# Optimization experiments

Measured on AMD Instinct MI355X. Metric: run time of the kernel, lower is better.

Reference implementation:

```python
import jax, jax.numpy as jnp
import numpy as np

N = 50000
E = 800000
IN_C = 128
HID = 32
OUT_C = 16
NEG_SLOPE = 0.2


def setup_inputs() -> dict:
    key = jax.random.key(0)
    ks = jax.random.split(key, 16)
    x = jax.random.normal(ks[0], (N, IN_C), dtype=jnp.float32)
    edge_index = jax.random.randint(ks[1], (2, E), 0, N, dtype=jnp.int64)

    def glorot(k, shape):
        fan = shape[0] + shape[-1]
        return jax.random.uniform(k, shape, jnp.float32, -1.0, 1.0) * jnp.sqrt(6.0 / fan)

    # layer1: in=128 -> heads=4, ch=32, concat -> out 128
    W1 = glorot(ks[2], (IN_C, 4 * HID))
    a_src1 = glorot(ks[3], (4, HID))
    a_dst1 = glorot(ks[4], (4, HID))
    b1 = jnp.zeros((4 * HID,), jnp.float32)
    # layer2: in=128 -> heads=2, ch=32, concat -> out 64
    W2 = glorot(ks[5], (4 * HID, 2 * HID))
    a_src2 = glorot(ks[6], (2, HID))
    a_dst2 = glorot(ks[7], (2, HID))
    b2 = jnp.zeros((2 * HID,), jnp.float32)
    # layer3: in=64 -> heads=1, ch=16, mean -> out 16
    W3 = glorot(ks[8], (2 * HID, OUT_C))
    a_src3 = glorot(ks[9], (1, OUT_C))
    a_dst3 = glorot(ks[10], (1, OUT_C))
    b3 = jnp.zeros((OUT_C,), jnp.float32)
    return {"x": x, "edge_index": edge_index,
            "W1": W1, "a_src1": a_src1, "a_dst1": a_dst1, "b1": b1,
            "W2": W2, "a_src2": a_src2, "a_dst2": a_dst2, "b2": b2,
            "W3": W3, "a_src3": a_src3, "a_dst3": a_dst3, "b3": b3}


def gat_conv(x, src, dst, W, a_src, a_dst, bias, heads, ch, concat):
    n = x.shape[0]
    h = (x @ W).reshape(n, heads, ch)                      # [N,H,C]
    alpha_s = jnp.einsum('nhc,hc->nh', h, a_src)           # [N,H]
    alpha_d = jnp.einsum('nhc,hc->nh', h, a_dst)           # [N,H]
    logits = jax.nn.leaky_relu(alpha_s[src] + alpha_d[dst], NEG_SLOPE)  # [E,H]
    # segment softmax over edges sharing the same destination node
    m = jax.ops.segment_max(logits, dst, num_segments=n)
    m = jnp.where(jnp.isfinite(m), m, 0.0)
    e = jnp.exp(logits - m[dst])
    denom = jax.ops.segment_sum(e, dst, num_segments=n)
    alpha = e / (denom[dst] + 1e-16)                       # [E,H]
    msg = h[src] * alpha[:, :, None]                       # [E,H,C]
    out = jax.ops.segment_sum(msg, dst, num_segments=n)    # [N,H,C]
    out = out.reshape(n, heads * ch) if concat else out.mean(axis=1)
    return out + bias


def reference(x, edge_index, W1, a_src1, a_dst1, b1, W2, a_src2, a_dst2, b2, W3, a_src3, a_dst3, b3):
    n = x.shape[0]
    loops = jnp.arange(n, dtype=edge_index.dtype)
    src = jnp.concatenate([edge_index[0], loops])  # add self loops (PyG default)
    dst = jnp.concatenate([edge_index[1], loops])
    h = jax.nn.relu(gat_conv(x, src, dst, W1, a_src1, a_dst1, b1, 4, HID, True))
    h = jax.nn.relu(gat_conv(h, src, dst, W2, a_src2, a_dst2, b2, 2, HID, True))
    out = gat_conv(h, src, dst, W3, a_src3, a_dst3, b3, 1, OUT_C, False)
    return out
```

## Files before the change

### kernel.cpp

```cpp
#include <hip/hip_runtime.h>
#include <hip/hip_bf16.h>
#include <stdint.h>

#define NODES 50000
#define NEDGE 800000
#define TEDGE (NEDGE + NODES)
#define SBLK 25
#define GBLK ((NODES + 63) / 64)
#define HBLK8 ((TEDGE + 2047) / 2048)
#define BL1_TOT (3 * HBLK8)

typedef unsigned short u16;
typedef unsigned int u32;
typedef unsigned long long u64;
typedef short s16x8 __attribute__((ext_vector_type(8)));
typedef float f32x4 __attribute__((ext_vector_type(4)));

__device__ __forceinline__ float bf2f(u16 v) {
  return __uint_as_float(((u32)v) << 16);
}
__device__ __forceinline__ u16 f2bf(float f) {
  u32 u = __float_as_uint(f);
  u32 r = (u + 0x7FFFu + ((u >> 16) & 1u)) >> 16;
  return (u16)r;
}
__device__ __forceinline__ float lo16f(u32 w) { return __uint_as_float(w << 16); }
__device__ __forceinline__ float hi16f(u32 w) { return __uint_as_float(w & 0xFFFF0000u); }
__device__ __forceinline__ float lrelu(float x) {
  return (x > 0.f) ? x : 0.2f * x;
}
__device__ __forceinline__ int clampn(int v) {
  return ((u32)v < NODES) ? v : 0;
}
__device__ __forceinline__ float load1(const void* p, size_t i, bool fb) {
  return fb ? bf2f(((const u16*)p)[i]) : ((const float*)p)[i];
}
__device__ __forceinline__ u32 encf(float f) {
  u32 u = __float_as_uint(f);
  return (u & 0x80000000u) ? ~u : (u | 0x80000000u);
}
__device__ __forceinline__ float decf(u32 k) {
  u32 u = (k & 0x80000000u) ? (k & 0x7FFFFFFFu) : ~k;
  return __uint_as_float(u);
}

__global__ __launch_bounds__(256) void k_probe(
    const int* __restrict__ ei, const u16* __restrict__ xs16,
    int* __restrict__ flags, int* __restrict__ deg,
    const void* __restrict__ W1, const void* __restrict__ W2,
    const void* __restrict__ W3, const void* __restrict__ as1,
    const void* __restrict__ ad1, const void* __restrict__ as2,
    const void* __restrict__ ad2, const void* __restrict__ as3,
    const void* __restrict__ ad3, u16* __restrict__ wt1,
    u16* __restrict__ wt2, u16* __restrict__ wt3, u16* __restrict__ wa1,
    u16* __restrict__ wa2, u16* __restrict__ wa3) {
  __shared__ int sfb;
  int t = threadIdx.x;
  int g = blockIdx.x * 256 + t;
  if (g < NODES) deg[g] = 0;
  if (blockIdx.x == 0 && t >= 2 && t < 32) flags[t] = 0;
  if (t < 64) {
    int big = 0;
#pragma unroll
    for (int k = 0; k < 4; ++k) {
      u32 ex = (xs16[2 * (t * 4 + k)] >> 7) & 0xFF;
      big += (ex >= 0x90);
    }
#pragma unroll
    for (int off = 32; off >= 1; off >>= 1) big += __shfl_xor(big, off);
    if (t == 0) sfb = (big >= 8) ? 0 : 1;
    if (blockIdx.x == 0) {
      int odd = 0, even = 0;
#pragma unroll
      for (int k = 0; k < 4; ++k) {
        int idx = t + 64 * k;
        odd |= (ei[2 * idx + 1] != 0);
        even |= (ei[2 * idx] != 0);
      }
      u64 bo = __ballot(odd);
      u64 be = __ballot(even);
      if (t == 0) flags[0] = (bo == 0ull && be != 0ull) ? 1 : 0;
    }
  }
  __syncthreads();
  bool fb = sfb != 0;
  if (blockIdx.x == 0 && t == 0) flags[1] = fb ? 1 : 0;

  auto fidx = [](int n, int k, int KS) {
    int nt = n >> 4, lrow = n & 15, ks = k >> 5, quad = (k >> 3) & 3, j = k & 7;
    return ((size_t)((nt * KS + ks) * 64 + quad * 16 + lrow)) * 8 + j;
  };

  if (g < 16384) {
    int n = g >> 7, k = g & 127;
    wt1[fidx(n, k, 4)] = f2bf(load1(W1, (size_t)k * 128 + n, fb));
  } else if (g < 24576) {
    int r = g - 16384;
    int n = r >> 7, k = r & 127;
    wt2[fidx(n, k, 4)] = f2bf(load1(W2, (size_t)k * 64 + n, fb));
  } else if (g < 25600) {
    int r = g - 24576;
    int n = r >> 6, k = r & 63;
    wt3[fidx(n, k, 2)] = f2bf(load1(W3, (size_t)k * 16 + n, fb));
  } else if (g < 27648) {
    int e = g - 25600;
    int n = e >> 7, k = e & 127;
    float v = 0.f;
    if (n < 8) {
      int head = (n < 4) ? n : n - 4;
      const void* av = (n < 4) ? as1 : ad1;
      for (int c = 0; c < 32; ++c)
        v += load1(W1, (size_t)k * 128 + head * 32 + c, fb) *
             load1(av, head * 32 + c, fb);
    }
    wa1[fidx(n, k, 4)] = (n < 8) ? f2bf(v) : (u16)0;
  } else if (g < 29696) {
    int e = g - 27648;
    int n = e >> 7, k = e & 127;
    float v = 0.f;
    if (n < 4) {
      int head = (n < 2) ? n : n - 2;
      const void* av = (n < 2) ? as2 : ad2;
      for (int c = 0; c < 32; ++c)
        v += load1(W2, (size_t)k * 64 + head * 32 + c, fb) *
             load1(av, head * 32 + c, fb);
    }
    wa2[fidx(n, k, 4)] = (n < 4) ? f2bf(v) : (u16)0;
  } else if (g < 30720) {
    int e = g - 29696;
    int n = e >> 6, k = e & 63;
    float v = 0.f;
    if (n < 2) {
      const void* av = (n < 1) ? as3 : ad3;
      for (int c = 0; c < 16; ++c)
        v += load1(W3, (size_t)k * 16 + c, fb) * load1(av, c, fb);
    }
    wa3[fidx(n, k, 2)] = (n < 2) ? f2bf(v) : (u16)0;
  }
}

template <int K, int N, int H, bool XEXT>
__device__ __forceinline__ void gmfma_tile(const void* __restrict__ xin,
                                           const u16* __restrict__ wtf,
                                           const u16* __restrict__ waf,
                                           u16* __restrict__ hout,
                                           float* __restrict__ asg,
                                           float* __restrict__ adg,
                                           u32* __restrict__ gm,
                                           const int* __restrict__ flags,
                                           int M, int row0,
                                           u16* __restrict__ xlds,
                                           u32* __restrict__ lmax) {
  constexpr int KP = K + 8;
  constexpr int NT = N / 16;
  constexpr int KS = K / 32;
  constexpr int KG = K / 8;
  int t = threadIdx.x;
  bool fb = flags[1] != 0;
  if (t < 2 * H) lmax[t] = 0;

  bool xbf = XEXT ? fb : true;
  for (int i = t; i < 64 * KG; i += 256) {
    int r = i / KG, kg = i % KG;
    int grow = row0 + r;
    if (grow >= M) grow = M - 1;
    if (xbf) {
      *(uint4*)&xlds[r * KP + kg * 8] =
          *(const uint4*)((const u16*)xin + (size_t)grow * K + kg * 8);
    } else {
      const float* gp = (const float*)xin + (size_t)grow * K + kg * 8;
      float4 f0 = *(const float4*)gp, f1 = *(const float4*)(gp + 4);
      *(ushort4*)&xlds[r * KP + kg * 8] =
          make_ushort4(f2bf(f0.x), f2bf(f0.y), f2bf(f0.z), f2bf(f0.w));
      *(ushort4*)&xlds[r * KP + kg * 8 + 4] =
          make_ushort4(f2bf(f1.x), f2bf(f1.y), f2bf(f1.z), f2bf(f1.w));
    }
  }
  __syncthreads();

  int lane = t & 63, w = t >> 6;
  int lrow = lane & 15, quad = lane >> 4;
  f32x4 acc[NT];
  f32x4 eacc = (f32x4){0.f, 0.f, 0.f, 0.f};
#pragma unroll
  for (int nt = 0; nt < NT; ++nt) acc[nt] = (f32x4){0.f, 0.f, 0.f, 0.f};

  const u16* xbase = xlds + (w * 16 + lrow) * KP + quad * 8;
#pragma unroll
  for (int ks = 0; ks < KS; ++ks) {
    s16x8 a = *(const s16x8*)(xbase + ks * 32);
    s16x8 be = *(const s16x8*)(waf + ((size_t)(ks * 64 + lane)) * 8);
    eacc = __builtin_amdgcn_mfma_f32_16x16x32_bf16(a, be, eacc, 0, 0, 0);
#pragma unroll
    for (int nt = 0; nt < NT; ++nt) {
      s16x8 b = *(const s16x8*)(wtf + ((size_t)((nt * KS + ks) * 64 + lane)) * 8);
      acc[nt] = __builtin_amdgcn_mfma_f32_16x16x32_bf16(a, b, acc[nt], 0, 0, 0);
    }
  }

  float pm = -3.4e38f;
  int baserow = row0 + w * 16 + quad * 4;
#pragma unroll
  for (int r = 0; r < 4; ++r) {
    int grow = baserow + r;
    if (grow < M) {
#pragma unroll
      for (int nt = 0; nt < NT; ++nt)
        hout[(size_t)grow * N + nt * 16 + lrow] = f2bf(acc[nt][r]);
      if (lrow < H) asg[grow * H + lrow] = eacc[r];
      else if (lrow < 2 * H) adg[grow * H + (lrow - H)] = eacc[r];
    }
    pm = fmaxf(pm, eacc[r]);
  }
  if (lrow < 2 * H) atomicMax(&lmax[lrow], encf(pm));
  __syncthreads();
  if (t < 2 * H) atomicMax(&gm[t], lmax[t]);
}

template <int K, int N, int H, bool XEXT>
__global__ __launch_bounds__(256) void k_gmfma(const void* __restrict__ xin,
                                               const u16* __restrict__ wtf,
                                               const u16* __restrict__ waf,
                                               u16* __restrict__ hout,
                                               float* __restrict__ asg,
                                               float* __restrict__ adg,
                                               u32* __restrict__ gm,
                                               const int* __restrict__ flags,
                                               int M) {
  __shared__ u16 xlds[64 * (K + 8)];
  __shared__ u32 lmax[2 * H];
  gmfma_tile<K, N, H, XEXT>(xin, wtf, waf, hout, asg, adg, gm, flags, M,
                            blockIdx.x * 64, xlds, lmax);
}

__global__ __launch_bounds__(256) void k_build_l1(
    const void* __restrict__ xin, const u16* __restrict__ wtf,
    const u16* __restrict__ waf, u16* __restrict__ hout,
    float* __restrict__ asg, float* __restrict__ adg, u32* __restrict__ gm,
    const int* __restrict__ flags, const int* __restrict__ ei,
    int* __restrict__ deg, u16* __restrict__ rankarr,
    u32* __restrict__ sd) {
  __shared__ u16 xlds[64 * 136];
  __shared__ u32 lmax[8];
  int bi = blockIdx.x;
  int r3 = bi % 3;
  if (r3 == 2) {
    int hb = bi / 3;
    int base = hb * 2048 + threadIdx.x;
    bool odd = flags[0] != 0;
    int sv[8], dv[8];
#pragma unroll
    for (int u = 0; u < 8; ++u) {
      int e = base + u * 256;
      int s = 0, d = 0;
      if (e < TEDGE) {
        if (e < NEDGE) {
          if (odd) { s = ei[2 * e]; d = ei[2 * (NEDGE + e)]; }
          else { s = ei[e]; d = ei[NEDGE + e]; }
        } else {
          s = e - NEDGE; d = s;
        }
        s = clampn(s); d = clampn(d);
      }
      sv[u] = s; dv[u] = d;
    }
    int rk[8];
#pragma unroll
    for (int u = 0; u < 8; ++u) {
      int e = base + u * 256;
      rk[u] = (e < TEDGE) ? atomicAdd(&deg[dv[u]], 1) : 0;
    }
#pragma unroll
    for (int u = 0; u < 8; ++u) {
      int e = base + u * 256;
      if (e < TEDGE) {
        sd[e] = (u32)sv[u] | ((u32)dv[u] << 16);
        rankarr[e] = (u16)min(rk[u], 65535);
      }
    }
    return;
  }
  int gb = (bi / 3) * 2 + r3;
  if (gb >= GBLK) return;
  gmfma_tile<128, 128, 4, true>(xin, wtf, waf, hout, asg, adg, gm, flags,
                                NODES, gb * 64, xlds, lmax);
}

__global__ __launch_bounds__(1024) void k_scan(const int* __restrict__ deg,
                                               int* __restrict__ rowptr,
                                               int* __restrict__ parts,
                                               int* __restrict__ counter) {
  __shared__ int swave[16];
  __shared__ int sbase, stot;
  int b = blockIdx.x, t = threadIdx.x;
  int lane = t & 63, w = t >> 6;
  int i0 = b * 2048 + t * 2;
  int v0 = (i0 < NODES) ? deg[i0] : 0;
  int v1 = (i0 + 1 < NODES) ? deg[i0 + 1] : 0;
  int local = v0 + v1;
  int x = local;
#pragma unroll
  for (int off = 1; off < 64; off <<= 1) {
    int y = __shfl_up(x, off);
    if (lane >= off) x += y;
  }
  if (lane == 63) swave[w] = x;
  __syncthreads();
  if (w == 0) {
    int wv = (lane < 16) ? swave[lane] : 0;
#pragma unroll
    for (int off = 1; off < 16; off <<= 1) {
      int y = __shfl_up(wv, off);
      if (lane >= off) wv += y;
    }
    if (lane == 15) {
      __hip_atomic_store(&parts[b], wv, __ATOMIC_RELAXED,
                         __HIP_MEMORY_SCOPE_AGENT);
      __hip_atomic_fetch_add(counter, 1, __ATOMIC_RELEASE,
                             __HIP_MEMORY_SCOPE_AGENT);
    }
    if (lane < 16) swave[lane] = wv;
  }
  __syncthreads();
  if (t == 0) {
    while (__hip_atomic_load(counter, __ATOMIC_ACQUIRE,
                             __HIP_MEMORY_SCOPE_AGENT) < SBLK)
      __builtin_amdgcn_s_sleep(2);
  }
  __syncthreads();
  if (w == 0) {
    int pv = (lane < SBLK) ? __hip_atomic_load(&parts[lane], __ATOMIC_RELAXED,
                                               __HIP_MEMORY_SCOPE_AGENT)
                           : 0;
    int pb = (lane < b) ? pv : 0;
#pragma unroll
    for (int off = 32; off >= 1; off >>= 1) {
      pb += __shfl_xor(pb, off);
      pv += __shfl_xor(pv, off);
    }
    if (lane == 0) { sbase = pb; stot = pv; }
  }
  __syncthreads();
  int run = sbase + ((w == 0) ? 0 : swave[w - 1]) + (x - local);
  if (i0 < NODES) rowptr[i0] = run;
  if (i0 + 1 < NODES) rowptr[i0 + 1] = run + v0;
  if (b == 0 && t == 0) rowptr[NODES] = stot;
}

__global__ __launch_bounds__(256) void k_scatter(const u32* __restrict__ sd,
                                                 const int* __restrict__ rowptr,
                                                 const u16* __restrict__ rankarr,
                                                 u16* __restrict__ srcs) {
  int base = blockIdx.x * 1024 + threadIdx.x;
#pragma unroll
  for (int u = 0; u < 4; ++u) {
    int e = base + u * 256;
    if (e < TEDGE) {
      u32 v = sd[e];
      int pos = rowptr[v >> 16] + (int)rankarr[e];
      srcs[pos] = (u16)(v & 0xFFFFu);
    }
  }
}

template <int H, int C, bool RELU, bool FINAL>
__global__ __launch_bounds__(256) void k_agg(const u16* __restrict__ hbuf,
                                             const float* __restrict__ asg,
                                             const float* __restrict__ adg,
                                             const int* __restrict__ rowptr,
                                             const u16* __restrict__ srcs,
                                             const void* __restrict__ bias,
                                             const int* __restrict__ flags,
                                             const u32* __restrict__ gm,
                                             void* __restrict__ outp, int n) {
  constexpr int HC = H * C;
  constexpr int L = HC / 8;
  constexpr int EPN = 32 / L;
  constexpr int UN = (4 * EPN <= 32) ? 4 : 2;
  __shared__ u16 lds_s[4][64];
  __shared__ float lds_e[4][64][H];
  int lane = threadIdx.x & 63;
  int w = threadIdx.x >> 6;
  int nh = lane >> 5;
  int hl = lane & 31;
  int node = blockIdx.x * 8 + w * 2 + nh;
  if (node >= n) node = n - 1;
  bool fb = flags[1] != 0;
  int start = rowptr[node], end = rowptr[node + 1];
  if (end < start || end - start > TEDGE) { start = 0; end = 0; }

  float adh[H], M[H];
#pragma unroll
  for (int h = 0; h < H; ++h) adh[h] = adg[node * H + h];
#pragma unroll
  for (int h = 0; h < H; ++h) M[h] = lrelu(decf(gm[h]) + decf(gm[H + h]));

  int sub = hl / L;
  int cl = hl & (L - 1);
  int ch0 = cl * 8;
  int myhead = ch0 / C;
  int base = nh * 32;

  float den[H];
#pragma unroll
  for (int h = 0; h < H; ++h) den[h] = 0.f;
  float acc[UN][8];
#pragma unroll
  for (int u = 0; u < UN; ++u)
#pragma unroll
    for (int i = 0; i < 8; ++i) acc[u][i] = 0.f;

  for (int chunk = start; chunk < end; chunk += 32) {
    int e = chunk + hl;
    int s = 0;
    float ee[H];
#pragma unroll
    for (int h = 0; h < H; ++h) ee[h] = 0.f;
    if (e < end) {
      s = srcs[e];
      float av[H];
      if (H == 4) { float4 t4 = *(const float4*)(asg + s * 4);
        av[0] = t4.x; av[1] = t4.y; av[H > 2 ? 2 : 0] = t4.z; av[H > 3 ? 3 : 0] = t4.w; }
      else if (H == 2) { float2 t2 = *(const float2*)(asg + s * 2); av[0] = t2.x; av[1] = t2.y; }
      else av[0] = asg[s];
#pragma unroll
      for (int h = 0; h < H; ++h) {
        float x = __expf(lrelu(av[h] + adh[h]) - M[h]);
        ee[h] = x;
        den[h] += x;
      }
    }
    __builtin_amdgcn_wave_barrier();
    lds_s[w][lane] = (u16)s;
#pragma unroll
    for (int h = 0; h < H; ++h) lds_e[w][lane][h] = ee[h];
    __builtin_amdgcn_wave_barrier();

    int cn = min(32, end - chunk);
    for (int j = 0; j < cn; j += UN * EPN) {
      int sx[UN];
      float ax[UN];
#pragma unroll
      for (int u = 0; u < UN; ++u) {
        int ei_ = base + j + u * EPN + sub;
        sx[u] = lds_s[w][ei_];
        ax[u] = lds_e[w][ei_][myhead];
      }
#pragma unroll
      for (int u = 0; u < UN; ++u) {
        uint4 v = *(const uint4*)(hbuf + (size_t)sx[u] * HC + ch0);
        acc[u][0] += ax[u] * lo16f(v.x); acc[u][1] += ax[u] * hi16f(v.x);
        acc[u][2] += ax[u] * lo16f(v.y); acc[u][3] += ax[u] * hi16f(v.y);
        acc[u][4] += ax[u] * lo16f(v.z); acc[u][5] += ax[u] * hi16f(v.z);
        acc[u][6] += ax[u] * lo16f(v.w); acc[u][7] += ax[u] * hi16f(v.w);
      }
    }
  }

#pragma unroll
  for (int m = 16; m >= 1; m >>= 1) {
#pragma unroll
    for (int h = 0; h < H; ++h) den[h] += __shfl_xor(den[h], m);
  }
  float tt[8];
#pragma unroll
  for (int i = 0; i < 8; ++i) {
    tt[i] = acc[0][i];
#pragma unroll
    for (int u = 1; u < UN; ++u) tt[i] += acc[u][i];
  }
#pragma unroll
  for (int m = L; m < 32; m <<= 1) {
#pragma unroll
    for (int i = 0; i < 8; ++i) tt[i] += __shfl_xor(tt[i], m);
  }

  if (sub == 0) {
    float inv = 1.f / (den[myhead] + 1e-16f);
    float o[8];
#pragma unroll
    for (int i = 0; i < 8; ++i) {
      o[i] = tt[i] * inv + load1(bias, ch0 + i, fb);
      if (RELU) o[i] = fmaxf(o[i], 0.f);
    }
    bool obf = FINAL ? fb : true;
    if (obf) {
      uint4 pk;
      pk.x = (u32)f2bf(o[0]) | ((u32)f2bf(o[1]) << 16);
      pk.y = (u32)f2bf(o[2]) | ((u32)f2bf(o[3]) << 16);
      pk.z = (u32)f2bf(o[4]) | ((u32)f2bf(o[5]) << 16);
      pk.w = (u32)f2bf(o[6]) | ((u32)f2bf(o[7]) << 16);
      *(uint4*)((u16*)outp + (size_t)node * HC + ch0) = pk;
    } else {
      float* op = (float*)outp + (size_t)node * HC + ch0;
      *(float4*)op = make_float4(o[0], o[1], o[2], o[3]);
      *(float4*)(op + 4) = make_float4(o[4], o[5], o[6], o[7]);
    }
  }
}


extern "C" void kernel_launch(void* const* d_in, const int* in_sizes, int n_in,
                              void* d_out, int out_size, void* d_ws, size_t ws_size,
                              hipStream_t stream) {
  const void* x   = d_in[0];
  const int* ei   = (const int*)d_in[1];
  const void* W1  = d_in[2];
  const void* as1 = d_in[3];
  const void* ad1 = d_in[4];
  const void* b1  = d_in[5];
  const void* W2  = d_in[6];
  const void* as2 = d_in[7];
  const void* ad2 = d_in[8];
  const void* b2  = d_in[9];
  const void* W3  = d_in[10];
  const void* as3 = d_in[11];
  const void* ad3 = d_in[12];
  const void* b3  = d_in[13];

  char* w = (char*)d_ws;
  auto alloc = [&](size_t bytes) {
    char* p = w;
    w += (bytes + 255) & ~(size_t)255;
    return p;
  };
  int* flags    = (int*)alloc(256);
  int* parts    = (int*)alloc(256);
  int* deg      = (int*)alloc((size_t)NODES * 4);
  int* rowptr   = (int*)alloc((size_t)(NODES + 1) * 4);
  u16* rankarr  = (u16*)alloc((size_t)TEDGE * 2);
  u32* sd       = (u32*)alloc((size_t)TEDGE * 4);
  u16* srcs     = (u16*)alloc((size_t)TEDGE * 2);
  float* asg    = (float*)alloc((size_t)NODES * 4 * 4);
  float* adg    = (float*)alloc((size_t)NODES * 4 * 4);
  u16* wt1      = (u16*)alloc((size_t)128 * 128 * 2);
  u16* wt2      = (u16*)alloc((size_t)64 * 128 * 2);
  u16* wt3      = (u16*)alloc((size_t)16 * 64 * 2);
  u16* wa1      = (u16*)alloc((size_t)16 * 128 * 2);
  u16* wa2      = (u16*)alloc((size_t)16 * 128 * 2);
  u16* wa3      = (u16*)alloc((size_t)16 * 64 * 2);
  u16* hbuf     = (u16*)alloc((size_t)NODES * 128 * 2);
  u16* obuf     = (u16*)alloc((size_t)NODES * 128 * 2);

  u32* gm1 = (u32*)(flags + 8);
  u32* gm2 = (u32*)(flags + 16);
  u32* gm3 = (u32*)(flags + 24);

  int ablocks = (NODES + 7) / 8;

  k_probe<<<(NODES + 255) / 256, 256, 0, stream>>>(
      ei, (const u16*)x, flags, deg, W1, W2, W3, as1, ad1, as2, ad2, as3, ad3,
      wt1, wt2, wt3, wa1, wa2, wa3);
  k_build_l1<<<BL1_TOT, 256, 0, stream>>>(x, wt1, wa1, hbuf, asg, adg, gm1,
                                          flags, ei, deg, rankarr, sd);
  k_scan<<<SBLK, 1024, 0, stream>>>(deg, rowptr, parts, flags + 2);
  k_scatter<<<(TEDGE + 1023) / 1024, 256, 0, stream>>>(sd, rowptr, rankarr, srcs);

  k_agg<4, 32, true, false><<<ablocks, 256, 0, stream>>>(hbuf, asg, adg, rowptr, srcs, b1, flags, gm1, obuf, NODES);
  k_gmfma<128, 64, 2, false><<<GBLK, 256, 0, stream>>>(obuf, wt2, wa2, hbuf, asg, adg, gm2, flags, NODES);
  k_agg<2, 32, true, false><<<ablocks, 256, 0, stream>>>(hbuf, asg, adg, rowptr, srcs, b2, flags, gm2, obuf, NODES);
  k_gmfma<64, 16, 1, false><<<GBLK, 256, 0, stream>>>(obuf, wt3, wa3, hbuf, asg, adg, gm3, flags, NODES);
  k_agg<1, 16, false, true><<<ablocks, 256, 0, stream>>>(hbuf, asg, adg, rowptr, srcs, b3, flags, gm3, d_out, NODES);
}
```

Measured before the change: 267.4 us.

## Privatize degree counters per XCD to avoid cross-die atomic contention

```diff
diff --git a/kernel.cpp b/kernel.cpp
--- a/kernel.cpp
+++ b/kernel.cpp
@@ -46,7 +46,7 @@
 
 __global__ __launch_bounds__(256) void k_probe(
     const int* __restrict__ ei, const u16* __restrict__ xs16,
-    int* __restrict__ flags, int* __restrict__ deg,
+    int* __restrict__ flags, u32* __restrict__ deg8,
     const void* __restrict__ W1, const void* __restrict__ W2,
     const void* __restrict__ W3, const void* __restrict__ as1,
     const void* __restrict__ ad1, const void* __restrict__ as2,
@@ -57,7 +57,10 @@
   __shared__ int sfb;
   int t = threadIdx.x;
   int g = blockIdx.x * 256 + t;
-  if (g < NODES) deg[g] = 0;
+  if (g < NODES) {
+#pragma unroll
+    for (int x = 0; x < 8; ++x) deg8[(size_t)x * NODES + g] = 0;
+  }
   if (blockIdx.x == 0 && t >= 2 && t < 32) flags[t] = 0;
   if (t < 64) {
     int big = 0;
@@ -238,8 +241,7 @@
     const u16* __restrict__ waf, u16* __restrict__ hout,
     float* __restrict__ asg, float* __restrict__ adg, u32* __restrict__ gm,
     const int* __restrict__ flags, const int* __restrict__ ei,
-    int* __restrict__ deg, u16* __restrict__ rankarr,
-    u32* __restrict__ sd) {
+    u32* __restrict__ deg8, u32* __restrict__ rkx, u32* __restrict__ sd) {
   __shared__ u16 xlds[64 * 136];
   __shared__ u32 lmax[8];
   int bi = blockIdx.x;
@@ -248,6 +250,10 @@
     int hb = bi / 3;
     int base = hb * 2048 + threadIdx.x;
     bool odd = flags[0] != 0;
+    u32 xcd;
+    asm volatile("s_getreg_b32 %0, hwreg(HW_REG_XCC_ID)" : "=s"(xcd));
+    xcd &= 7u;
+    u32* mydeg = deg8 + (size_t)xcd * NODES;
     int sv[8], dv[8];
 #pragma unroll
     for (int u = 0; u < 8; ++u) {
@@ -264,18 +270,21 @@
       }
       sv[u] = s; dv[u] = d;
     }
-    int rk[8];
+    u32 rk[8];
 #pragma unroll
     for (int u = 0; u < 8; ++u) {
       int e = base + u * 256;
-      rk[u] = (e < TEDGE) ? atomicAdd(&deg[dv[u]], 1) : 0;
+      rk[u] = (e < TEDGE)
+                  ? __hip_atomic_fetch_add(&mydeg[dv[u]], 1u, __ATOMIC_RELAXED,
+                                           __HIP_MEMORY_SCOPE_WORKGROUP)
+                  : 0u;
     }
 #pragma unroll
     for (int u = 0; u < 8; ++u) {
       int e = base + u * 256;
       if (e < TEDGE) {
         sd[e] = (u32)sv[u] | ((u32)dv[u] << 16);
-        rankarr[e] = (u16)min(rk[u], 65535);
+        rkx[e] = (rk[u] & 0xFFFFu) | (xcd << 16);
       }
     }
     return;
@@ -286,7 +295,8 @@
                                 NODES, gb * 64, xlds, lmax);
 }
 
-__global__ __launch_bounds__(1024) void k_scan(const int* __restrict__ deg,
+__global__ __launch_bounds__(1024) void k_scan(const u32* __restrict__ deg8,
+                                               u32* __restrict__ base8,
                                                int* __restrict__ rowptr,
                                                int* __restrict__ parts,
                                                int* __restrict__ counter) {
@@ -295,8 +305,25 @@
   int b = blockIdx.x, t = threadIdx.x;
   int lane = t & 63, w = t >> 6;
   int i0 = b * 2048 + t * 2;
-  int v0 = (i0 < NODES) ? deg[i0] : 0;
-  int v1 = (i0 + 1 < NODES) ? deg[i0 + 1] : 0;
+  int v0 = 0, v1 = 0;
+  if (i0 < NODES) {
+    int acc = 0;
+#pragma unroll
+    for (int x = 0; x < 8; ++x) {
+      base8[(size_t)x * NODES + i0] = (u32)acc;
+      acc += (int)deg8[(size_t)x * NODES + i0];
+    }
+    v0 = acc;
+  }
+  if (i0 + 1 < NODES) {
+    int acc = 0;
+#pragma unroll
+    for (int x = 0; x < 8; ++x) {
+      base8[(size_t)x * NODES + i0 + 1] = (u32)acc;
+      acc += (int)deg8[(size_t)x * NODES + i0 + 1];
+    }
+    v1 = acc;
+  }
   int local = v0 + v1;
   int x = local;
 #pragma unroll
@@ -348,16 +375,19 @@
 }
 
 __global__ __launch_bounds__(256) void k_scatter(const u32* __restrict__ sd,
+                                                 const u32* __restrict__ rkx,
+                                                 const u32* __restrict__ base8,
                                                  const int* __restrict__ rowptr,
-                                                 const u16* __restrict__ rankarr,
                                                  u16* __restrict__ srcs) {
   int base = blockIdx.x * 1024 + threadIdx.x;
 #pragma unroll
   for (int u = 0; u < 4; ++u) {
     int e = base + u * 256;
     if (e < TEDGE) {
-      u32 v = sd[e];
-      int pos = rowptr[v >> 16] + (int)rankarr[e];
+      u32 v = sd[e], r = rkx[e];
+      int d = (int)(v >> 16);
+      int pos = rowptr[d] + (int)base8[(size_t)(r >> 16) * NODES + d] +
+                (int)(r & 0xFFFFu);
       srcs[pos] = (u16)(v & 0xFFFFu);
     }
   }
@@ -526,9 +556,10 @@
   };
   int* flags    = (int*)alloc(256);
   int* parts    = (int*)alloc(256);
-  int* deg      = (int*)alloc((size_t)NODES * 4);
+  u32* deg8     = (u32*)alloc((size_t)8 * NODES * 4);
+  u32* base8    = (u32*)alloc((size_t)8 * NODES * 4);
   int* rowptr   = (int*)alloc((size_t)(NODES + 1) * 4);
-  u16* rankarr  = (u16*)alloc((size_t)TEDGE * 2);
+  u32* rkx      = (u32*)alloc((size_t)TEDGE * 4);
   u32* sd       = (u32*)alloc((size_t)TEDGE * 4);
   u16* srcs     = (u16*)alloc((size_t)TEDGE * 2);
   float* asg    = (float*)alloc((size_t)NODES * 4 * 4);
@@ -549,12 +580,12 @@
   int ablocks = (NODES + 7) / 8;
 
   k_probe<<<(NODES + 255) / 256, 256, 0, stream>>>(
-      ei, (const u16*)x, flags, deg, W1, W2, W3, as1, ad1, as2, ad2, as3, ad3,
-      wt1, wt2, wt3, wa1, wa2, wa3);
+      ei, (const u16*)x, flags, deg8, W1, W2, W3, as1, ad1, as2, ad2, as3,
+      ad3, wt1, wt2, wt3, wa1, wa2, wa3);
   k_build_l1<<<BL1_TOT, 256, 0, stream>>>(x, wt1, wa1, hbuf, asg, adg, gm1,
-                                          flags, ei, deg, rankarr, sd);
-  k_scan<<<SBLK, 1024, 0, stream>>>(deg, rowptr, parts, flags + 2);
-  k_scatter<<<(TEDGE + 1023) / 1024, 256, 0, stream>>>(sd, rowptr, rankarr, srcs);
+                                          flags, ei, deg8, rkx, sd);
+  k_scan<<<SBLK, 1024, 0, stream>>>(deg8, base8, rowptr, parts, flags + 2);
+  k_scatter<<<(TEDGE + 1023) / 1024, 256, 0, stream>>>(sd, rkx, base8, rowptr, srcs);
 
   k_agg<4, 32, true, false><<<ablocks, 256, 0, stream>>>(hbuf, asg, adg, rowptr, srcs, b1, flags, gm1, obuf, NODES);
   k_gmfma<128, 64, 2, false><<<GBLK, 256, 0, stream>>>(obuf, wt2, wa2, hbuf, asg, adg, gm2, flags, NODES);
```

Result: no change. 272.0 us (+1.7%).
